# Optimization experiments

Hardware: AMD Instinct MI355X
Metric: run time of the kernel (lower is better)

## Reference

```python
import jax, jax.numpy as jnp
import numpy as np

ORDER = 4


def setup_inputs() -> dict:
    key = jax.random.key(0)
    k1, k2, k3, k4 = jax.random.split(key, 4)
    B, IN, OUT = 8192, 1024, 1024
    x = jax.random.normal(k1, (B, IN), dtype=jnp.float32)
    base_weight = jax.random.normal(k2, (OUT, IN), dtype=jnp.float32) * (1.0 / np.sqrt(IN))
    std = 1.0 / (IN * np.sqrt(ORDER))
    taylor_coeffs = jax.random.normal(k3, (OUT, IN, ORDER), dtype=jnp.float32) * std
    bound = 1.0 / np.sqrt(IN)
    bias = jax.random.uniform(k4, (OUT,), dtype=jnp.float32, minval=-bound, maxval=bound)
    return {"x": x, "base_weight": base_weight, "taylor_coeffs": taylor_coeffs, "bias": bias}


def reference(x, base_weight, taylor_coeffs, bias):
    # base path: SiLU(x) @ W^T
    base_out = jnp.einsum('bi,oi->bo', jax.nn.silu(x), base_weight)
    # taylor path: x_powers[b,i,k] = x**k, k=0..ORDER-1; contract with coeffs[o,i,k]
    powers = jnp.arange(ORDER, dtype=x.dtype)  # [K]
    x_powers = x[:, :, None] ** powers  # [B, IN, K]
    taylor_out = jnp.einsum('bik,oik->bo', x_powers, taylor_coeffs)
    return base_out + taylor_out + bias
```

## Files before the change

### kernel.cpp

```cpp
#include <hip/hip_runtime.h>
#include <hip/hip_bf16.h>

#define GLOBAL_AS __attribute__((address_space(1)))
#define LDS_AS    __attribute__((address_space(3)))

typedef __bf16 bf16x8 __attribute__((ext_vector_type(8)));
typedef float  f32x4  __attribute__((ext_vector_type(4)));

constexpr int BATCH = 8192;
constexpr int IN    = 1024;
constexpr int OUT   = 1024;
constexpr int KDIM  = IN * 4;
constexpr int BM = 128, BN = 256, BK = 64;
constexpr int NKT  = KDIM / BK;
constexpr int LDSBUF = 24576;

__device__ __forceinline__ unsigned short f2bf(float f) {
    union { float f; unsigned u; } v; v.f = f;
    unsigned r = v.u + 0x7fffu + ((v.u >> 16) & 1u);
    return (unsigned short)(r >> 16);
}
__device__ __forceinline__ unsigned pk(unsigned short a, unsigned short b) {
    return (unsigned)a | ((unsigned)b << 16);
}

__global__ __launch_bounds__(256) void prep(const float* __restrict__ x,
                                            const float* __restrict__ W,
                                            const float* __restrict__ C,
                                            const float* __restrict__ bias,
                                            unsigned short* __restrict__ Ab,
                                            unsigned short* __restrict__ Bb,
                                            float* __restrict__ be) {
    if (blockIdx.x < 8192) {
        int idx = blockIdx.x * 256 + threadIdx.x;
        float4 v = reinterpret_cast<const float4*>(x)[idx];
        float e0[4] = {v.x, v.y, v.z, v.w};
        unsigned short o[16];
#pragma unroll
        for (int j = 0; j < 4; ++j) {
            float xv = e0[j];
            float s  = xv / (1.0f + __expf(-xv));
            float x2 = xv * xv;
            o[4*j+0] = f2bf(s);
            o[4*j+1] = f2bf(xv);
            o[4*j+2] = f2bf(x2);
            o[4*j+3] = f2bf(x2 * xv);
        }
        uint4 d0 = make_uint4(pk(o[0],o[1]), pk(o[2],o[3]),   pk(o[4],o[5]),   pk(o[6],o[7]));
        uint4 d1 = make_uint4(pk(o[8],o[9]), pk(o[10],o[11]), pk(o[12],o[13]), pk(o[14],o[15]));
        uint4* dst = reinterpret_cast<uint4*>(Ab) + (size_t)idx * 2;
        dst[0] = d0;
        dst[1] = d1;
    } else {
        const int o = blockIdx.x - 8192, t = threadIdx.x;
        const int i0 = t * 4;
        const float4* c4 = reinterpret_cast<const float4*>(C + ((size_t)o * IN + i0) * 4);
        float4 w4 = *reinterpret_cast<const float4*>(W + (size_t)o * IN + i0);
        float wv[4] = {w4.x, w4.y, w4.z, w4.w};
        float s = 0.f;
        unsigned d[8];
#pragma unroll
        for (int j = 0; j < 4; ++j) {
            float4 c = c4[j];
            s += c.x;
            d[2*j]   = pk(f2bf(wv[j]), f2bf(c.y));
            d[2*j+1] = pk(f2bf(c.z),   f2bf(c.w));
        }
        uint4* dst = reinterpret_cast<uint4*>(Bb + (size_t)o * KDIM + i0 * 4);
        dst[0] = make_uint4(d[0], d[1], d[2], d[3]);
        dst[1] = make_uint4(d[4], d[5], d[6], d[7]);
#pragma unroll
        for (int off = 32; off > 0; off >>= 1) s += __shfl_down(s, off, 64);
        __shared__ float red[4];
        if ((t & 63) == 0) red[t >> 6] = s;
        __syncthreads();
        if (t == 0) be[o] = bias[o] + red[0] + red[1] + red[2] + red[3];
    }
}

__global__ __launch_bounds__(512, 2) void gemm_kan(
        const unsigned short* __restrict__ Ab,
        const unsigned short* __restrict__ Bb,
        const float* __restrict__ be,
        float* __restrict__ out) {
    extern __shared__ unsigned short smem[];

    const int t    = threadIdx.x;
    const int l    = blockIdx.x;
    const int xcd  = l & 7;
    const int bn   = xcd >> 1;
    const int bm   = (xcd & 1) * 32 + (l >> 3);
    const int lane = t & 63;
    const int wave = t >> 6;
    const int wr   = wave >> 2;
    const int wc   = wave & 3;
    const int l15  = lane & 15;
    const int quad = lane >> 4;
    const int x7   = l15 & 7;

    const int rowT = t >> 3;
    const int chT  = (t & 7) ^ (rowT & 7);
    const unsigned short* aS = Ab + (size_t)(bm * BM + rowT) * KDIM + chT * 8;
    const unsigned short* bS = Bb + (size_t)(bn * BN + rowT) * KDIM + chT * 8;

    const int aRd = (wr * 32 + l15) * 64;
    const int bRd = 8192 + (wc * 64 + l15) * 64;
    const int ck0 = (quad ^ x7) * 8;
    const int ck1 = ((4 + quad) ^ x7) * 8;

    f32x4 acc[4][4];
    const f32x4 zero = {0.f, 0.f, 0.f, 0.f};
#pragma unroll
    for (int i = 0; i < 4; ++i)
#pragma unroll
        for (int j = 0; j < 4; ++j) acc[i][j] = zero;

#define STAGE_A(tile, buf, h)                                                          \
    __builtin_amdgcn_global_load_lds(                                                  \
        (const GLOBAL_AS void*)(aS + (size_t)(tile) * BK + (size_t)(h) * 64 * KDIM),   \
        (LDS_AS void*)(smem + (buf) * LDSBUF + (h) * 4096 + t * 8), 16, 0, 0)

#define STAGE_B(tile, buf, h) do {                                                     \
    const unsigned short* s_ = bS + (size_t)(tile) * BK + (size_t)(h) * 128 * KDIM;    \
    unsigned short* d_ = smem + (buf) * LDSBUF + 8192 + (h) * 8192 + t * 8;            \
    __builtin_amdgcn_global_load_lds((const GLOBAL_AS void*)s_, (LDS_AS void*)d_,      \
                                     16, 0, 0);                                        \
    __builtin_amdgcn_global_load_lds((const GLOBAL_AS void*)(s_ + (size_t)64 * KDIM),  \
                                     (LDS_AS void*)(d_ + 4096), 16, 0, 0);             \
} while (0)

    STAGE_A(0, 0, 0); STAGE_B(0, 0, 0); STAGE_A(0, 0, 1); STAGE_B(0, 0, 1);
    STAGE_A(1, 1, 0); STAGE_B(1, 1, 0); STAGE_A(1, 1, 1); STAGE_B(1, 1, 1);
    asm volatile("s_waitcnt vmcnt(6)" ::: "memory");
    __builtin_amdgcn_s_barrier();

    int cb = 0;
    for (int kt = 0; kt < NKT; ++kt) {
        const unsigned short* sb = smem + cb * LDSBUF;
        const int  nb = (cb >= 1) ? cb - 1 : 2;
        const bool pf = (kt + 2) < NKT;

        bf16x8 av[2][2], bvv[4][2];

        av[0][0] = *reinterpret_cast<const bf16x8*>(sb + aRd + ck0);
        av[0][1] = *reinterpret_cast<const bf16x8*>(sb + aRd + ck1);
        av[1][0] = *reinterpret_cast<const bf16x8*>(sb + aRd + 1024 + ck0);
        av[1][1] = *reinterpret_cast<const bf16x8*>(sb + aRd + 1024 + ck1);
#pragma unroll
        for (int ni = 0; ni < 4; ++ni) {
            bvv[ni][0] = *reinterpret_cast<const bf16x8*>(sb + bRd + ni * 1024 + ck0);
            bvv[ni][1] = *reinterpret_cast<const bf16x8*>(sb + bRd + ni * 1024 + ck1);
        }
        if (pf) { STAGE_A(kt + 2, nb, 0); STAGE_B(kt + 2, nb, 0); }
        __builtin_amdgcn_s_barrier();
        asm volatile("s_waitcnt lgkmcnt(0)" ::: "memory");
        __builtin_amdgcn_sched_barrier(0);
        __builtin_amdgcn_s_setprio(1);
#pragma unroll
        for (int kk = 0; kk < 2; ++kk)
#pragma unroll
            for (int mi = 0; mi < 2; ++mi)
#pragma unroll
                for (int ni = 0; ni < 4; ++ni)
                    acc[mi][ni] = __builtin_amdgcn_mfma_f32_16x16x32_bf16(
                        av[mi][kk], bvv[ni][kk], acc[mi][ni], 0, 0, 0);
        __builtin_amdgcn_s_setprio(0);
        __builtin_amdgcn_s_barrier();

        av[0][0] = *reinterpret_cast<const bf16x8*>(sb + aRd + 4096 + ck0);
        av[0][1] = *reinterpret_cast<const bf16x8*>(sb + aRd + 4096 + ck1);
        av[1][0] = *reinterpret_cast<const bf16x8*>(sb + aRd + 5120 + ck0);
        av[1][1] = *reinterpret_cast<const bf16x8*>(sb + aRd + 5120 + ck1);
        if (pf) { STAGE_A(kt + 2, nb, 1); STAGE_B(kt + 2, nb, 1); }
        __builtin_amdgcn_s_barrier();
        asm volatile("s_waitcnt lgkmcnt(0)" ::: "memory");
        __builtin_amdgcn_sched_barrier(0);
        __builtin_amdgcn_s_setprio(1);
#pragma unroll
        for (int kk = 0; kk < 2; ++kk)
#pragma unroll
            for (int mi = 0; mi < 2; ++mi)
#pragma unroll
                for (int ni = 0; ni < 4; ++ni)
                    acc[2 + mi][ni] = __builtin_amdgcn_mfma_f32_16x16x32_bf16(
                        av[mi][kk], bvv[ni][kk], acc[2 + mi][ni], 0, 0, 0);
        __builtin_amdgcn_s_setprio(0);

        if (kt < NKT - 2) {
            asm volatile("s_waitcnt vmcnt(6)" ::: "memory");
            __builtin_amdgcn_s_barrier();
        } else if (kt == NKT - 2) {
            asm volatile("s_waitcnt vmcnt(0)" ::: "memory");
            __builtin_amdgcn_s_barrier();
        }
        cb = (cb == 2) ? 0 : cb + 1;
    }

#undef STAGE_A
#undef STAGE_B

    float bev[4];
#pragma unroll
    for (int ni = 0; ni < 4; ++ni)
        bev[ni] = be[bn * BN + wc * 64 + ni * 16 + l15];

#pragma unroll
    for (int mg = 0; mg < 4; ++mg) {
        const int grow = bm * BM + (mg >> 1) * 64 + wr * 32 + (mg & 1) * 16 + quad * 4;
#pragma unroll
        for (int ni = 0; ni < 4; ++ni) {
            const int gcol = bn * BN + wc * 64 + ni * 16 + l15;
            float* po = out + (size_t)grow * OUT + gcol;
#pragma unroll
            for (int r = 0; r < 4; ++r)
                po[(size_t)r * OUT] = acc[mg][ni][r] + bev[ni];
        }
    }
}

extern "C" void kernel_launch(void* const* d_in, const int* in_sizes, int n_in,
                              void* d_out, int out_size, void* d_ws, size_t ws_size,
                              hipStream_t stream) {
    const float* x    = (const float*)d_in[0];
    const float* W    = (const float*)d_in[1];
    const float* C    = (const float*)d_in[2];
    const float* bias = (const float*)d_in[3];
    float* out = (float*)d_out;

    unsigned short* Ab = (unsigned short*)d_ws;
    unsigned short* Bb = Ab + (size_t)BATCH * KDIM;
    float*          be = (float*)(Bb + (size_t)OUT * KDIM);

    constexpr int LDS_BYTES = 3 * LDSBUF * 2;
    static bool inited = false;
    if (!inited) {
        hipFuncSetAttribute(reinterpret_cast<const void*>(&gemm_kan),
                            hipFuncAttributeMaxDynamicSharedMemorySize, LDS_BYTES);
        inited = true;
    }

    prep<<<dim3(8192 + 1024), dim3(256), 0, stream>>>(x, W, C, bias, Ab, Bb, be);

    gemm_kan<<<dim3(256), dim3(512), LDS_BYTES, stream>>>(Ab, Bb, be, out);
}
```

Measured before the change: 176.9 us.

## Fuse activation feature expansion into GEMM A-tile staging from raw x

The prep kernel no longer writes an expanded bf16 A matrix (SiLU, x, x^2, x^3) to global memory. The GEMM now loads fp32 x directly, computes the four features in registers and writes them into swizzled LDS, prefetching two tiles ahead as before. This removes a large global write and re-read of the expanded activations. In exchange the main loop gains per-tile exp, divide and conversion work plus synchronous LDS stores, and x features are recomputed by each of the four column blocks.

```diff
diff --git a/kernel.cpp b/kernel.cpp
--- a/kernel.cpp
+++ b/kernel.cpp
@@ -24,62 +24,38 @@
     return (unsigned)a | ((unsigned)b << 16);
 }
 
-__global__ __launch_bounds__(256) void prep(const float* __restrict__ x,
-                                            const float* __restrict__ W,
-                                            const float* __restrict__ C,
-                                            const float* __restrict__ bias,
-                                            unsigned short* __restrict__ Ab,
-                                            unsigned short* __restrict__ Bb,
-                                            float* __restrict__ be) {
-    if (blockIdx.x < 8192) {
-        int idx = blockIdx.x * 256 + threadIdx.x;
-        float4 v = reinterpret_cast<const float4*>(x)[idx];
-        float e0[4] = {v.x, v.y, v.z, v.w};
-        unsigned short o[16];
-#pragma unroll
-        for (int j = 0; j < 4; ++j) {
-            float xv = e0[j];
-            float s  = xv / (1.0f + __expf(-xv));
-            float x2 = xv * xv;
-            o[4*j+0] = f2bf(s);
-            o[4*j+1] = f2bf(xv);
-            o[4*j+2] = f2bf(x2);
-            o[4*j+3] = f2bf(x2 * xv);
-        }
-        uint4 d0 = make_uint4(pk(o[0],o[1]), pk(o[2],o[3]),   pk(o[4],o[5]),   pk(o[6],o[7]));
-        uint4 d1 = make_uint4(pk(o[8],o[9]), pk(o[10],o[11]), pk(o[12],o[13]), pk(o[14],o[15]));
-        uint4* dst = reinterpret_cast<uint4*>(Ab) + (size_t)idx * 2;
-        dst[0] = d0;
-        dst[1] = d1;
-    } else {
-        const int o = blockIdx.x - 8192, t = threadIdx.x;
-        const int i0 = t * 4;
-        const float4* c4 = reinterpret_cast<const float4*>(C + ((size_t)o * IN + i0) * 4);
-        float4 w4 = *reinterpret_cast<const float4*>(W + (size_t)o * IN + i0);
-        float wv[4] = {w4.x, w4.y, w4.z, w4.w};
-        float s = 0.f;
-        unsigned d[8];
-#pragma unroll
-        for (int j = 0; j < 4; ++j) {
-            float4 c = c4[j];
-            s += c.x;
-            d[2*j]   = pk(f2bf(wv[j]), f2bf(c.y));
-            d[2*j+1] = pk(f2bf(c.z),   f2bf(c.w));
-        }
-        uint4* dst = reinterpret_cast<uint4*>(Bb + (size_t)o * KDIM + i0 * 4);
-        dst[0] = make_uint4(d[0], d[1], d[2], d[3]);
-        dst[1] = make_uint4(d[4], d[5], d[6], d[7]);
-#pragma unroll
-        for (int off = 32; off > 0; off >>= 1) s += __shfl_down(s, off, 64);
-        __shared__ float red[4];
-        if ((t & 63) == 0) red[t >> 6] = s;
-        __syncthreads();
-        if (t == 0) be[o] = bias[o] + red[0] + red[1] + red[2] + red[3];
-    }
+__global__ __launch_bounds__(256) void prep_b(const float* __restrict__ W,
+                                              const float* __restrict__ C,
+                                              const float* __restrict__ bias,
+                                              unsigned short* __restrict__ Bb,
+                                              float* __restrict__ be) {
+    const int o = blockIdx.x, t = threadIdx.x;
+    const int i0 = t * 4;
+    const float4* c4 = reinterpret_cast<const float4*>(C + ((size_t)o * IN + i0) * 4);
+    float4 w4 = *reinterpret_cast<const float4*>(W + (size_t)o * IN + i0);
+    float wv[4] = {w4.x, w4.y, w4.z, w4.w};
+    float s = 0.f;
+    unsigned d[8];
+#pragma unroll
+    for (int j = 0; j < 4; ++j) {
+        float4 c = c4[j];
+        s += c.x;
+        d[2*j]   = pk(f2bf(wv[j]), f2bf(c.y));
+        d[2*j+1] = pk(f2bf(c.z),   f2bf(c.w));
+    }
+    uint4* dst = reinterpret_cast<uint4*>(Bb + (size_t)o * KDIM + i0 * 4);
+    dst[0] = make_uint4(d[0], d[1], d[2], d[3]);
+    dst[1] = make_uint4(d[4], d[5], d[6], d[7]);
+#pragma unroll
+    for (int off = 32; off > 0; off >>= 1) s += __shfl_down(s, off, 64);
+    __shared__ float red[4];
+    if ((t & 63) == 0) red[t >> 6] = s;
+    __syncthreads();
+    if (t == 0) be[o] = bias[o] + red[0] + red[1] + red[2] + red[3];
 }
 
 __global__ __launch_bounds__(512, 2) void gemm_kan(
-        const unsigned short* __restrict__ Ab,
+        const float* __restrict__ x,
         const unsigned short* __restrict__ Bb,
         const float* __restrict__ be,
         float* __restrict__ out) {
@@ -100,8 +76,14 @@
 
     const int rowT = t >> 3;
     const int chT  = (t & 7) ^ (rowT & 7);
-    const unsigned short* aS = Ab + (size_t)(bm * BM + rowT) * KDIM + chT * 8;
     const unsigned short* bS = Bb + (size_t)(bn * BN + rowT) * KDIM + chT * 8;
+
+    const int arow   = t >> 2;
+    const int axi    = t & 3;
+    const int aoff0  = arow * 64 + (((axi * 2)     ^ (arow & 7)) * 8);
+    const int aoff1  = arow * 64 + (((axi * 2 + 1) ^ (arow & 7)) * 8);
+    const float4* xp = reinterpret_cast<const float4*>(
+        x + (size_t)(bm * BM + arow) * IN + axi * 4);
 
     const int aRd = (wr * 32 + l15) * 64;
     const int bRd = 8192 + (wc * 64 + l15) * 64;
@@ -114,11 +96,6 @@
     for (int i = 0; i < 4; ++i)
 #pragma unroll
         for (int j = 0; j < 4; ++j) acc[i][j] = zero;
-
-#define STAGE_A(tile, buf, h)                                                          \
-    __builtin_amdgcn_global_load_lds(                                                  \
-        (const GLOBAL_AS void*)(aS + (size_t)(tile) * BK + (size_t)(h) * 64 * KDIM),   \
-        (LDS_AS void*)(smem + (buf) * LDSBUF + (h) * 4096 + t * 8), 16, 0, 0)
 
 #define STAGE_B(tile, buf, h) do {                                                     \
     const unsigned short* s_ = bS + (size_t)(tile) * BK + (size_t)(h) * 128 * KDIM;    \
@@ -129,9 +106,33 @@
                                      (LDS_AS void*)(d_ + 4096), 16, 0, 0);             \
 } while (0)
 
-    STAGE_A(0, 0, 0); STAGE_B(0, 0, 0); STAGE_A(0, 0, 1); STAGE_B(0, 0, 1);
-    STAGE_A(1, 1, 0); STAGE_B(1, 1, 0); STAGE_A(1, 1, 1); STAGE_B(1, 1, 1);
-    asm volatile("s_waitcnt vmcnt(6)" ::: "memory");
+#define STAGE_A(buf, v) do {                                                           \
+    float e_[4] = {(v).x, (v).y, (v).z, (v).w};                                        \
+    unsigned short o_[16];                                                             \
+    _Pragma("unroll")                                                                  \
+    for (int j = 0; j < 4; ++j) {                                                      \
+        float xv_ = e_[j];                                                             \
+        float s_  = xv_ / (1.0f + __expf(-xv_));                                       \
+        float x2_ = xv_ * xv_;                                                         \
+        o_[4*j+0] = f2bf(s_);                                                          \
+        o_[4*j+1] = f2bf(xv_);                                                         \
+        o_[4*j+2] = f2bf(x2_);                                                         \
+        o_[4*j+3] = f2bf(x2_ * xv_);                                                   \
+    }                                                                                  \
+    unsigned short* ab_ = smem + (buf) * LDSBUF;                                       \
+    *reinterpret_cast<uint4*>(ab_ + aoff0) =                                           \
+        make_uint4(pk(o_[0],o_[1]), pk(o_[2],o_[3]), pk(o_[4],o_[5]), pk(o_[6],o_[7]));\
+    *reinterpret_cast<uint4*>(ab_ + aoff1) =                                           \
+        make_uint4(pk(o_[8],o_[9]), pk(o_[10],o_[11]), pk(o_[12],o_[13]), pk(o_[14],o_[15]));\
+} while (0)
+
+    float4 xa = xp[0];
+    STAGE_B(0, 0, 0); STAGE_B(0, 0, 1);
+    float4 xb = xp[4];
+    STAGE_B(1, 1, 0); STAGE_B(1, 1, 1);
+    STAGE_A(0, xa);
+    STAGE_A(1, xb);
+    asm volatile("s_waitcnt vmcnt(4) lgkmcnt(0)" ::: "memory");
     __builtin_amdgcn_s_barrier();
 
     int cb = 0;
@@ -141,6 +142,7 @@
         const bool pf = (kt + 2) < NKT;
 
         bf16x8 av[2][2], bvv[4][2];
+        float4 xv = {0.f, 0.f, 0.f, 0.f};
 
         av[0][0] = *reinterpret_cast<const bf16x8*>(sb + aRd + ck0);
         av[0][1] = *reinterpret_cast<const bf16x8*>(sb + aRd + ck1);
@@ -151,7 +153,7 @@
             bvv[ni][0] = *reinterpret_cast<const bf16x8*>(sb + bRd + ni * 1024 + ck0);
             bvv[ni][1] = *reinterpret_cast<const bf16x8*>(sb + bRd + ni * 1024 + ck1);
         }
-        if (pf) { STAGE_A(kt + 2, nb, 0); STAGE_B(kt + 2, nb, 0); }
+        if (pf) { xv = xp[(kt + 2) * 4]; STAGE_B(kt + 2, nb, 0); }
         __builtin_amdgcn_s_barrier();
         asm volatile("s_waitcnt lgkmcnt(0)" ::: "memory");
         __builtin_amdgcn_sched_barrier(0);
@@ -171,7 +173,10 @@
         av[0][1] = *reinterpret_cast<const bf16x8*>(sb + aRd + 4096 + ck1);
         av[1][0] = *reinterpret_cast<const bf16x8*>(sb + aRd + 5120 + ck0);
         av[1][1] = *reinterpret_cast<const bf16x8*>(sb + aRd + 5120 + ck1);
-        if (pf) { STAGE_A(kt + 2, nb, 1); STAGE_B(kt + 2, nb, 1); }
+        if (pf) {
+            STAGE_B(kt + 2, nb, 1);
+            STAGE_A(nb, xv);
+        }
         __builtin_amdgcn_s_barrier();
         asm volatile("s_waitcnt lgkmcnt(0)" ::: "memory");
         __builtin_amdgcn_sched_barrier(0);
@@ -187,7 +192,7 @@
         __builtin_amdgcn_s_setprio(0);
 
         if (kt < NKT - 2) {
-            asm volatile("s_waitcnt vmcnt(6)" ::: "memory");
+            asm volatile("s_waitcnt vmcnt(4)" ::: "memory");
             __builtin_amdgcn_s_barrier();
         } else if (kt == NKT - 2) {
             asm volatile("s_waitcnt vmcnt(0)" ::: "memory");
@@ -227,8 +232,7 @@
     const float* bias = (const float*)d_in[3];
     float* out = (float*)d_out;
 
-    unsigned short* Ab = (unsigned short*)d_ws;
-    unsigned short* Bb = Ab + (size_t)BATCH * KDIM;
+    unsigned short* Bb = (unsigned short*)d_ws;
     float*          be = (float*)(Bb + (size_t)OUT * KDIM);
 
     constexpr int LDS_BYTES = 3 * LDSBUF * 2;
@@ -239,7 +243,7 @@
         inited = true;
     }
 
-    prep<<<dim3(8192 + 1024), dim3(256), 0, stream>>>(x, W, C, bias, Ab, Bb, be);
-
-    gemm_kan<<<dim3(256), dim3(512), LDS_BYTES, stream>>>(Ab, Bb, be, out);
-}
+    prep_b<<<dim3(1024), dim3(256), 0, stream>>>(W, C, bias, Bb, be);
+
+    gemm_kan<<<dim3(256), dim3(512), LDS_BYTES, stream>>>(x, Bb, be, out);
+}
```

New measurement: 203.5 us. 1.15x slower.

## Simplify GEMM main loop to single-phase staging and drop XCD-aware block mapping

Applied to the files above, without the earlier changes.

Replaces the two-half ping-pong schedule, with its intermediate barriers, setprio and split prefetch, by a single prefetch of the whole next-next tile at the top of each iteration, followed by two k-substeps that each load A and B fragments from LDS and issue 16 MFMAs. Source pointers are precomputed per thread. Block-to-tile mapping changes from an XCD-grouped swizzle to a plain row-major bm/bn split. This cuts barriers and scheduling constraints, but risks less overlap of LDS reads with MFMA and worse L2 locality across XCDs.

```diff
diff --git a/kernel.cpp b/kernel.cpp
--- a/kernel.cpp
+++ b/kernel.cpp
@@ -87,9 +87,8 @@
 
     const int t    = threadIdx.x;
     const int l    = blockIdx.x;
-    const int xcd  = l & 7;
-    const int bn   = xcd >> 1;
-    const int bm   = (xcd & 1) * 32 + (l >> 3);
+    const int bm   = l & 63;
+    const int bn   = l >> 6;
     const int lane = t & 63;
     const int wave = t >> 6;
     const int wr   = wave >> 2;
@@ -98,15 +97,21 @@
     const int quad = lane >> 4;
     const int x7   = l15 & 7;
 
-    const int rowT = t >> 3;
-    const int chT  = (t & 7) ^ (rowT & 7);
-    const unsigned short* aS = Ab + (size_t)(bm * BM + rowT) * KDIM + chT * 8;
-    const unsigned short* bS = Bb + (size_t)(bn * BN + rowT) * KDIM + chT * 8;
+    const unsigned short* aP[2];
+    const unsigned short* bP[4];
+#pragma unroll
+    for (int i = 0; i < 2; ++i) {
+        int ch = i * 512 + t, r = ch >> 3, g = (ch & 7) ^ (r & 7);
+        aP[i] = Ab + (size_t)(bm * BM + r) * KDIM + g * 8;
+    }
+#pragma unroll
+    for (int i = 0; i < 4; ++i) {
+        int ch = i * 512 + t, r = ch >> 3, g = (ch & 7) ^ (r & 7);
+        bP[i] = Bb + (size_t)(bn * BN + r) * KDIM + g * 8;
+    }
 
     const int aRd = (wr * 32 + l15) * 64;
     const int bRd = 8192 + (wc * 64 + l15) * 64;
-    const int ck0 = (quad ^ x7) * 8;
-    const int ck1 = ((4 + quad) ^ x7) * 8;
 
     f32x4 acc[4][4];
     const f32x4 zero = {0.f, 0.f, 0.f, 0.f};
@@ -115,76 +120,50 @@
 #pragma unroll
         for (int j = 0; j < 4; ++j) acc[i][j] = zero;
 
-#define STAGE_A(tile, buf, h)                                                          \
-    __builtin_amdgcn_global_load_lds(                                                  \
-        (const GLOBAL_AS void*)(aS + (size_t)(tile) * BK + (size_t)(h) * 64 * KDIM),   \
-        (LDS_AS void*)(smem + (buf) * LDSBUF + (h) * 4096 + t * 8), 16, 0, 0)
-
-#define STAGE_B(tile, buf, h) do {                                                     \
-    const unsigned short* s_ = bS + (size_t)(tile) * BK + (size_t)(h) * 128 * KDIM;    \
-    unsigned short* d_ = smem + (buf) * LDSBUF + 8192 + (h) * 8192 + t * 8;            \
-    __builtin_amdgcn_global_load_lds((const GLOBAL_AS void*)s_, (LDS_AS void*)d_,      \
-                                     16, 0, 0);                                        \
-    __builtin_amdgcn_global_load_lds((const GLOBAL_AS void*)(s_ + (size_t)64 * KDIM),  \
-                                     (LDS_AS void*)(d_ + 4096), 16, 0, 0);             \
+#define STAGE(tile, buf) do {                                                          \
+    _Pragma("unroll")                                                                  \
+    for (int i_ = 0; i_ < 2; ++i_)                                                     \
+        __builtin_amdgcn_global_load_lds(                                              \
+            (const GLOBAL_AS void*)(aP[i_] + (size_t)(tile) * BK),                     \
+            (LDS_AS void*)(smem + (buf) * LDSBUF + (i_ * 512 + t) * 8), 16, 0, 0);     \
+    _Pragma("unroll")                                                                  \
+    for (int i_ = 0; i_ < 4; ++i_)                                                     \
+        __builtin_amdgcn_global_load_lds(                                              \
+            (const GLOBAL_AS void*)(bP[i_] + (size_t)(tile) * BK),                     \
+            (LDS_AS void*)(smem + (buf) * LDSBUF + 8192 + (i_ * 512 + t) * 8),         \
+            16, 0, 0);                                                                 \
 } while (0)
 
-    STAGE_A(0, 0, 0); STAGE_B(0, 0, 0); STAGE_A(0, 0, 1); STAGE_B(0, 0, 1);
-    STAGE_A(1, 1, 0); STAGE_B(1, 1, 0); STAGE_A(1, 1, 1); STAGE_B(1, 1, 1);
+    STAGE(0, 0);
+    STAGE(1, 1);
     asm volatile("s_waitcnt vmcnt(6)" ::: "memory");
     __builtin_amdgcn_s_barrier();
 
     int cb = 0;
     for (int kt = 0; kt < NKT; ++kt) {
         const unsigned short* sb = smem + cb * LDSBUF;
-        const int  nb = (cb >= 1) ? cb - 1 : 2;
-        const bool pf = (kt + 2) < NKT;
-
-        bf16x8 av[2][2], bvv[4][2];
-
-        av[0][0] = *reinterpret_cast<const bf16x8*>(sb + aRd + ck0);
-        av[0][1] = *reinterpret_cast<const bf16x8*>(sb + aRd + ck1);
-        av[1][0] = *reinterpret_cast<const bf16x8*>(sb + aRd + 1024 + ck0);
-        av[1][1] = *reinterpret_cast<const bf16x8*>(sb + aRd + 1024 + ck1);
-#pragma unroll
-        for (int ni = 0; ni < 4; ++ni) {
-            bvv[ni][0] = *reinterpret_cast<const bf16x8*>(sb + bRd + ni * 1024 + ck0);
-            bvv[ni][1] = *reinterpret_cast<const bf16x8*>(sb + bRd + ni * 1024 + ck1);
-        }
-        if (pf) { STAGE_A(kt + 2, nb, 0); STAGE_B(kt + 2, nb, 0); }
-        __builtin_amdgcn_s_barrier();
-        asm volatile("s_waitcnt lgkmcnt(0)" ::: "memory");
-        __builtin_amdgcn_sched_barrier(0);
-        __builtin_amdgcn_s_setprio(1);
-#pragma unroll
-        for (int kk = 0; kk < 2; ++kk)
-#pragma unroll
-            for (int mi = 0; mi < 2; ++mi)
+        const int nb = (cb >= 1) ? cb - 1 : 2;
+
+        if (kt + 2 < NKT) STAGE(kt + 2, nb);
+
+#pragma unroll
+        for (int kk = 0; kk < 2; ++kk) {
+            const int ck = ((kk * 4 + quad) ^ x7) * 8;
+            bf16x8 af[4], bv[4];
+            af[0] = *reinterpret_cast<const bf16x8*>(sb + aRd + ck);
+            af[1] = *reinterpret_cast<const bf16x8*>(sb + aRd + 1024 + ck);
+            af[2] = *reinterpret_cast<const bf16x8*>(sb + aRd + 4096 + ck);
+            af[3] = *reinterpret_cast<const bf16x8*>(sb + aRd + 5120 + ck);
+#pragma unroll
+            for (int ni = 0; ni < 4; ++ni)
+                bv[ni] = *reinterpret_cast<const bf16x8*>(sb + bRd + ni * 1024 + ck);
+#pragma unroll
+            for (int mi = 0; mi < 4; ++mi)
 #pragma unroll
                 for (int ni = 0; ni < 4; ++ni)
                     acc[mi][ni] = __builtin_amdgcn_mfma_f32_16x16x32_bf16(
-                        av[mi][kk], bvv[ni][kk], acc[mi][ni], 0, 0, 0);
-        __builtin_amdgcn_s_setprio(0);
-        __builtin_amdgcn_s_barrier();
-
-        av[0][0] = *reinterpret_cast<const bf16x8*>(sb + aRd + 4096 + ck0);
-        av[0][1] = *reinterpret_cast<const bf16x8*>(sb + aRd + 4096 + ck1);
-        av[1][0] = *reinterpret_cast<const bf16x8*>(sb + aRd + 5120 + ck0);
-        av[1][1] = *reinterpret_cast<const bf16x8*>(sb + aRd + 5120 + ck1);
-        if (pf) { STAGE_A(kt + 2, nb, 1); STAGE_B(kt + 2, nb, 1); }
-        __builtin_amdgcn_s_barrier();
-        asm volatile("s_waitcnt lgkmcnt(0)" ::: "memory");
-        __builtin_amdgcn_sched_barrier(0);
-        __builtin_amdgcn_s_setprio(1);
-#pragma unroll
-        for (int kk = 0; kk < 2; ++kk)
-#pragma unroll
-            for (int mi = 0; mi < 2; ++mi)
-#pragma unroll
-                for (int ni = 0; ni < 4; ++ni)
-                    acc[2 + mi][ni] = __builtin_amdgcn_mfma_f32_16x16x32_bf16(
-                        av[mi][kk], bvv[ni][kk], acc[2 + mi][ni], 0, 0, 0);
-        __builtin_amdgcn_s_setprio(0);
+                        af[mi], bv[ni], acc[mi][ni], 0, 0, 0);
+        }
 
         if (kt < NKT - 2) {
             asm volatile("s_waitcnt vmcnt(6)" ::: "memory");
@@ -196,8 +175,7 @@
         cb = (cb == 2) ? 0 : cb + 1;
     }
 
-#undef STAGE_A
-#undef STAGE_B
+#undef STAGE
 
     float bev[4];
 #pragma unroll
```

Result: faster. 173.2 us (-2.0%).
